# Optimization experiments

Hardware: AMD Instinct MI355X
Metric: run time of the kernel (lower is better)

The kernel has to match this reference:

```python
import jax, jax.numpy as jnp
import numpy as np

N = 250_000          # total event nodes across the batch
E = 1_000_000        # directed edges (radius-graph style, avg degree 4)
B = 25               # graphs in the batch
BS = N // B          # nodes per graph (contiguous blocks)
NX, NY = 8, 9        # ceil(120/16), ceil(100/12) voxel cells for MaxPooling
NC = NX * NY         # 72 voxel cells per graph
M = B * NC           # pooled node slots (empty cells kept but masked)
GRIDS = 16           # MaxPoolingX: 4x4 cells of size (30,25) over 120x100
NOUT = 2
EPS = 1e-5


def spline_basis(p):
    # SplineConv basis: kernel_size=2 per dim, degree=1 open B-spline, dim=3.
    # basis_s(p) = prod_d (p_d if bit_d(s) else 1 - p_d), s = b0 + 2*b1 + 4*b2
    p = jnp.clip(p, 0.0, 1.0)
    cols = []
    for s in range(8):
        w = jnp.ones(p.shape[0], p.dtype)
        for d in range(3):
            w = w * (p[:, d] if (s >> d) & 1 else 1.0 - p[:, d])
        cols.append(w)
    return jnp.stack(cols, axis=1)  # [E, 8]


def spline_conv(x, src, dst, basis, W, emask, num_nodes):
    # SplineConv with aggr='mean', bias=False, root_weight=False
    xj = x[src]                                   # [E, Cin] gather
    msg = jnp.zeros((xj.shape[0], W.shape[2]), x.dtype)
    for s in range(W.shape[0]):                   # 8 kernel weight matrices
        msg = msg + basis[:, s:s + 1] * (xj @ W[s])
    msg = msg * emask[:, None]
    out = jax.ops.segment_sum(msg, dst, num_segments=num_nodes)
    deg = jax.ops.segment_sum(emask, dst, num_segments=num_nodes)
    return out / jnp.maximum(deg, 1.0)[:, None]


def batch_norm(x, gamma, beta, mask=None):
    # BatchNorm1d over nodes (training-mode batch statistics, biased var)
    if mask is None:
        mean = x.mean(axis=0)
        var = jnp.mean((x - mean) ** 2, axis=0)
        return (x - mean) * jax.lax.rsqrt(var + EPS) * gamma + beta
    m = mask.astype(x.dtype)[:, None]
    cnt = jnp.maximum(m.sum(), 1.0)
    mean = (x * m).sum(axis=0) / cnt
    var = (((x - mean) ** 2) * m).sum(axis=0) / cnt
    return ((x - mean) * jax.lax.rsqrt(var + EPS) * gamma + beta) * m


def _forward(x, pos, edge_attr, ws, gs, bs, fc_w, edge_index, batch):
    src, dst = edge_index[0], edge_index[1]
    basis = spline_basis(edge_attr)
    em = jnp.ones((src.shape[0],), x.dtype)
    for i in range(5):  # conv1..conv5 + norm + relu on the full event graph
        x = spline_conv(x, src, dst, basis, ws[i], em, N)
        x = jax.nn.relu(batch_norm(x, gs[i], bs[i]))
    # ---- MaxPooling: voxel grid (16,12) over pos[:, :2], coarsen graph ----
    cx = jnp.clip(jnp.floor(pos[:, 0] / 16.0).astype(jnp.int32), 0, NX - 1)
    cy = jnp.clip(jnp.floor(pos[:, 1] / 12.0).astype(jnp.int32), 0, NY - 1)
    cluster = batch * NC + cy * NX + cx           # [N] -> [0, M)
    cnt = jax.ops.segment_sum(jnp.ones((N,), x.dtype), cluster, num_segments=M)
    nmask = cnt > 0                               # non-empty voxel cells
    xp = jax.ops.segment_max(x, cluster, num_segments=M)
    xp = jnp.where(nmask[:, None], xp, 0.0)       # [M, 32]
    pp = jax.ops.segment_sum(pos, cluster, num_segments=M) / jnp.maximum(cnt, 1.0)[:, None]
    # coarsen edges: remap via cluster, drop self loops, coalesce duplicates
    key = cluster[src] * M + cluster[dst]
    key = jnp.where(cluster[src] == cluster[dst], M * M, key)
    ks = jnp.sort(key)
    dup = jnp.concatenate([jnp.zeros((1,), bool), ks[1:] == ks[:-1]])
    evalid = (ks < M * M) & (~dup)
    rs = jnp.where(evalid, ks // M, 0)
    cs = jnp.where(evalid, ks % M, 0)
    emf = evalid.astype(x.dtype)
    # Cartesian(norm=True, cat=False) on pooled positions
    d = (pp[cs] - pp[rs]) * emf[:, None]
    maxv = jnp.maximum(jnp.max(jnp.abs(d)), 1e-9)
    ea2 = d / (2.0 * maxv) + 0.5
    basis2 = spline_basis(ea2)
    for i in range(5, 7):  # conv6, conv7 on pooled graph
        xp = spline_conv(xp, rs, cs, basis2, ws[i], emf, M)
        xp = jax.nn.relu(batch_norm(xp, gs[i], bs[i], nmask))
    # ---- MaxPoolingX: (30,25) voxel grid -> 4x4 = 16 cells per graph ----
    bcl = jnp.arange(M, dtype=jnp.int32) // NC    # batch id of each cluster
    gx = jnp.clip(jnp.floor(pp[:, 0] / 30.0).astype(jnp.int32), 0, 3)
    gy = jnp.clip(jnp.floor(pp[:, 1] / 25.0).astype(jnp.int32), 0, 3)
    seg = jnp.where(nmask, bcl * GRIDS + gy * 4 + gx, B * GRIDS)
    xg = jax.ops.segment_max(xp, seg, num_segments=B * GRIDS + 1)[:B * GRIDS]
    xg = jnp.where(jnp.isfinite(xg), xg, 0.0)     # empty cells -> 0
    feat = xg.reshape(B, GRIDS * 32)              # [B, 512]
    return feat @ fc_w.T                          # [B, NOUT]


def setup_inputs() -> dict:
    key = jax.random.key(0)
    k = jax.random.split(key, 16)
    x = jax.random.uniform(k[0], (N, 1), dtype=jnp.float32)
    pos = jax.random.uniform(k[1], (N, 3), dtype=jnp.float32) * jnp.array([120.0, 100.0, 1.0], jnp.float32)
    batch = (jnp.arange(N) // BS).astype(jnp.int32)
    src = jax.random.randint(k[2], (E,), 0, N, dtype=jnp.int32)
    dst = (src // BS) * BS + jax.random.randint(k[3], (E,), 0, BS, dtype=jnp.int32)
    edge_index = jnp.stack([src, dst])
    edge_attr = jax.random.uniform(k[4], (E, 3), dtype=jnp.float32)
    chans = [1, 8, 16, 16, 16, 32, 32, 32]
    inp = {"x": x, "pos": pos, "edge_attr": edge_attr}
    for i in range(7):
        cin, cout = chans[i], chans[i + 1]
        inp[f"w{i+1}"] = jax.random.normal(k[5 + i], (8, cin, cout), jnp.float32) / np.sqrt(8.0 * cin)
    for i in range(7):
        inp[f"g{i+1}"] = jnp.ones((chans[i + 1],), jnp.float32)
    for i in range(7):
        inp[f"b{i+1}"] = jnp.zeros((chans[i + 1],), jnp.float32)
    inp["fc_w"] = jax.random.normal(k[12], (NOUT, GRIDS * 32), jnp.float32) * 0.05
    inp["edge_index"] = edge_index
    inp["batch"] = batch
    return inp


def reference(x, pos, edge_attr, w1, w2, w3, w4, w5, w6, w7,
              g1, g2, g3, g4, g5, g6, g7,
              b1, b2, b3, b4, b5, b6, b7, fc_w, edge_index, batch):
    ws = (w1, w2, w3, w4, w5, w6, w7)
    gs = (g1, g2, g3, g4, g5, g6, g7)
    bs = (b1, b2, b3, b4, b5, b6, b7)
    return _forward(x, pos, edge_attr, ws, gs, bs, fc_w, edge_index, batch)
```

## Files before the change

kernel.cpp:

```cpp
#include <hip/hip_runtime.h>

constexpr int NN   = 250000;
constexpr int NE   = 1000000;
constexpr int NBm  = 25;
constexpr int BSg  = NN / NBm;
constexpr int NCc  = 72;
constexpr int MM   = NBm * NCc;
constexpr int PRES = NBm * NCc * NCc;
constexpr int NBK  = NBm * 16;
constexpr float EPSbn = 1e-5f;


__global__ __launch_bounds__(256) void k_deg(const int* __restrict__ dst, int* __restrict__ deg, int n) {
    int e = blockIdx.x * 256 + threadIdx.x;
    if (e < n) atomicAdd(&deg[dst[e]], 1);
}

__global__ __launch_bounds__(256) void k_dhist(const int* __restrict__ deg, const int* __restrict__ batch,
                                               int* __restrict__ dhist, int n) {
    __shared__ int h[NBK];
    int tid = threadIdx.x;
    for (int i = tid; i < NBK; i += 256) h[i] = 0;
    __syncthreads();
    int i = blockIdx.x * 256 + tid;
    if (i < n) atomicAdd(&h[batch[i] * 16 + (15 - min(deg[i], 15))], 1);
    __syncthreads();
    for (int b = tid; b < NBK; b += 256) if (h[b]) atomicAdd(&dhist[b], h[b]);
}

__global__ __launch_bounds__(256) void k_dscan(const int* __restrict__ dhist, int* __restrict__ dcur) {
    __shared__ int tmp[NBK];
    int t = threadIdx.x;
    for (int i = t; i < NBK; i += 256) tmp[i] = dhist[i];
    __syncthreads();
    if (t == 0) { int run = 0; for (int i = 0; i < NBK; i++) { int v = tmp[i]; tmp[i] = run; run += v; } }
    __syncthreads();
    for (int i = t; i < NBK; i += 256) dcur[i] = tmp[i];
}

__global__ __launch_bounds__(256) void k_dscat(const int* __restrict__ deg, const int* __restrict__ batch,
                                               const float* __restrict__ x_in,
                                               int* __restrict__ dcur, int* __restrict__ pinv,
                                               int* __restrict__ deg_p, float* __restrict__ xin_p, int n) {
    __shared__ int lcnt[NBK];
    __shared__ int gbase[NBK];
    int tid = threadIdx.x;
    for (int i = tid; i < NBK; i += 256) lcnt[i] = 0;
    __syncthreads();
    int i = blockIdx.x * 256 + tid;
    int b = 0, rank = 0;
    if (i < n) {
        b = batch[i] * 16 + (15 - min(deg[i], 15));
        rank = atomicAdd(&lcnt[b], 1);
    }
    __syncthreads();
    for (int k = tid; k < NBK; k += 256)
        if (lcnt[k]) gbase[k] = atomicAdd(&dcur[k], lcnt[k]);
    __syncthreads();
    if (i < n) {
        int slot = gbase[b] + rank;
        pinv[i] = slot;
        deg_p[slot] = deg[i];
        xin_p[slot] = x_in[i];
    }
}

__global__ __launch_bounds__(256) void k_scan1(const int* __restrict__ in, int n,
                                               int* __restrict__ outEx, int* __restrict__ bsum) {
    __shared__ int lds[256];
    int t = threadIdx.x;
    int base = blockIdx.x * 2048;
    int v[8]; int s = 0;
#pragma unroll
    for (int i = 0; i < 8; i++) { int idx = base + t * 8 + i; v[i] = (idx < n) ? in[idx] : 0; s += v[i]; }
    lds[t] = s; __syncthreads();
    for (int o = 1; o < 256; o <<= 1) {
        int x = (t >= o) ? lds[t - o] : 0; __syncthreads();
        lds[t] += x; __syncthreads();
    }
    if (t == 255) bsum[blockIdx.x] = lds[255];
    int run = lds[t] - s;
#pragma unroll
    for (int i = 0; i < 8; i++) { int idx = base + t * 8 + i; if (idx < n) outEx[idx] = run; run += v[i]; }
}

__global__ __launch_bounds__(256) void k_scan2(int* bsum, int nb) {
    __shared__ int l[256];
    int t = threadIdx.x;
    int v = (t < nb) ? bsum[t] : 0;
    l[t] = v; __syncthreads();
    for (int o = 1; o < 256; o <<= 1) {
        int x = (t >= o) ? l[t - o] : 0; __syncthreads();
        l[t] += x; __syncthreads();
    }
    if (t < nb) bsum[t] = l[t] - v;
}

__global__ __launch_bounds__(256) void k_scan3(int* __restrict__ outEx, int n, const int* __restrict__ bsum) {
    int i = blockIdx.x * 256 + threadIdx.x;
    if (i < n) outEx[i] += bsum[i >> 11];
}

__global__ __launch_bounds__(256) void k_scatter(const int* __restrict__ src, const int* __restrict__ dst,
                                                 const float* __restrict__ ea, const int* __restrict__ offx,
                                                 const int* __restrict__ pinv,
                                                 int* __restrict__ cursor, float4* __restrict__ erec, int n) {
    int e = blockIdx.x * 256 + threadIdx.x;
    if (e >= n) return;
    int d = pinv[dst[e]];
    int j = offx[d] + atomicAdd(&cursor[d], 1);
    float p0 = fminf(fmaxf(ea[e * 3 + 0], 0.f), 1.f);
    float p1 = fminf(fmaxf(ea[e * 3 + 1], 0.f), 1.f);
    float p2 = fminf(fmaxf(ea[e * 3 + 2], 0.f), 1.f);
    erec[j] = make_float4(__int_as_float(pinv[src[e]]), p0, p1, p2);
}

__global__ __launch_bounds__(256) void k_cluster(const float* __restrict__ pos, const int* __restrict__ batch,
                                                 const int* __restrict__ pinv,
                                                 int* __restrict__ cluster, int* __restrict__ cluster_p,
                                                 int* __restrict__ cnt, float* __restrict__ ppsum, int n) {
    int i = blockIdx.x * 256 + threadIdx.x;
    if (i >= n) return;
    float px = pos[i * 3], py = pos[i * 3 + 1], pz = pos[i * 3 + 2];
    int cx = min(max((int)floorf(px / 16.f), 0), 7);
    int cy = min(max((int)floorf(py / 12.f), 0), 8);
    int cl = batch[i] * NCc + cy * 8 + cx;
    cluster[i] = cl;
    cluster_p[pinv[i]] = cl;
    atomicAdd(&cnt[cl], 1);
    atomicAdd(&ppsum[cl * 3 + 0], px);
    atomicAdd(&ppsum[cl * 3 + 1], py);
    atomicAdd(&ppsum[cl * 3 + 2], pz);
}

__global__ __launch_bounds__(256) void k_coarse(const int* __restrict__ src, const int* __restrict__ dst,
                                                const int* __restrict__ cluster, unsigned char* __restrict__ presence,
                                                int n) {
    int e = blockIdx.x * 256 + threadIdx.x;
    if (e >= n) return;
    int r = cluster[src[e]], c = cluster[dst[e]];
    if (r == c) return;
    int g = r / NCc;
    presence[g * (NCc * NCc) + (r % NCc) * NCc + (c % NCc)] = 1;
}

__global__ __launch_bounds__(256) void k_fpp(const int* __restrict__ cnt, const float* __restrict__ ppsum,
                                             float* __restrict__ pp, int* __restrict__ nmask, int* __restrict__ nmc) {
    int m = blockIdx.x * 256 + threadIdx.x;
    if (m >= MM) return;
    int c = cnt[m];
    float inv = 1.f / (float)max(c, 1);
    pp[m * 3 + 0] = ppsum[m * 3 + 0] * inv;
    pp[m * 3 + 1] = ppsum[m * 3 + 1] * inv;
    pp[m * 3 + 2] = ppsum[m * 3 + 2] * inv;
    nmask[m] = (c > 0);
    if (c > 0) atomicAdd(nmc, 1);
}

__global__ __launch_bounds__(256) void k_maxv(const unsigned char* __restrict__ presence, const float* __restrict__ pp,
                                              float* __restrict__ maxv) {
    int i = blockIdx.x * 256 + threadIdx.x;
    float m = 0.f;
    if (i < PRES && presence[i]) {
        int g = i / (NCc * NCc), rem = i % (NCc * NCc);
        int r = g * NCc + rem / NCc, c = g * NCc + rem % NCc;
        float d0 = fabsf(pp[c * 3 + 0] - pp[r * 3 + 0]);
        float d1 = fabsf(pp[c * 3 + 1] - pp[r * 3 + 1]);
        float d2 = fabsf(pp[c * 3 + 2] - pp[r * 3 + 2]);
        m = fmaxf(fmaxf(d0, d1), d2);
    }
    for (int o = 32; o; o >>= 1) m = fmaxf(m, __shfl_xor(m, o));
    if ((threadIdx.x & 63) == 0) atomicMax((int*)maxv, __float_as_int(m));
}


template <int CIN, int COUT, int TPN, bool BN>
__global__ __launch_bounds__(256) void k_conv(
    const float* __restrict__ x, const float4* __restrict__ erec,
    const int* __restrict__ off, const int* __restrict__ deg,
    const float* __restrict__ W, const float* __restrict__ st,
    const float* __restrict__ gam, const float* __restrict__ bet, float invcnt,
    float* __restrict__ out, float* __restrict__ stG, int nwaves) {
    constexpr int CPT = CIN / TPN;
    constexpr int SLICE = COUT + 4;
    constexpr int NPW = 128 / TPN;
    constexpr int CPG = (BSg + NPW - 1) / NPW;
    constexpr int WPG = (CPG + 1) / 2;
    constexpr int NH = (COUT > 16) ? 2 : 1;
    constexpr int OH = COUT / NH;
    constexpr int CWH = OH / TPN;
    __shared__ float Ws[8 * CIN * SLICE];
    __shared__ float ssum[COUT], ssq[COUT];
    int tid = threadIdx.x;
    for (int idx = tid; idx < 8 * CIN * COUT; idx += 256) {
        int s = idx / (CIN * COUT), r = idx % (CIN * COUT);
        int ci = r / COUT, co = r % COUT;
        int t_ = ci / CPT, i_ = ci % CPT;
        Ws[((s * CPT + i_) * TPN + t_) * SLICE + co] = W[idx];
    }
    if (tid < COUT) { ssum[tid] = 0.f; ssq[tid] = 0.f; }
    __syncthreads();

    int w = blockIdx.x * 4 + (tid >> 6);
    int lane = tid & 63;
    int t = lane & (TPN - 1);
    int qi = lane / TPN;
    bool wact = (w < nwaves);
    int g = wact ? (w / WPG) : 0;
    int p = wact ? (w % WPG) : 0;

    float sc[CPT], sh[CPT];
    if constexpr (BN) {
#pragma unroll
        for (int i = 0; i < CPT; i++) {
            int c = t * CPT + i;
            float mean = st[c] * invcnt;
            float var = st[CIN + c] * invcnt - mean * mean;
            float s = rsqrtf(var + EPSbn) * gam[c];
            sc[i] = s; sh[i] = bet[c] - mean * s;
        }
    }

    for (int rep = 0; rep < 2; rep++) {
        if (!wact) break;
        int c = rep ? (CPG - 1 - p) : p;
        if (rep && c == p) break;
        int base = g * BSg + c * NPW;
        int lim = min(NPW, BSg - c * NPW);
        int no = 2 * qi;
        bool act = no < lim;
        int n0 = base + no;

        float agg[2][8 * CPT];
#pragma unroll
        for (int r = 0; r < 2; r++)
#pragma unroll
            for (int i = 0; i < 8 * CPT; i++) agg[r][i] = 0.f;

        int dgr[2] = {0, 0};
        int jbr[2] = {0, 0};
        if (act) {
            jbr[0] = off[n0];     dgr[0] = deg[n0];
            jbr[1] = off[n0 + 1]; dgr[1] = deg[n0 + 1];
        }
        int mx = max(dgr[0], dgr[1]);
        for (int m = 0; m < mx; m++) {
#pragma unroll
            for (int r = 0; r < 2; r++) {
                if (m < dgr[r]) {
                    float4 rec = erec[jbr[r] + m];
                    int s = __float_as_int(rec.x);
                    float p0 = rec.y, p1 = rec.z, p2 = rec.w;
                    float q0 = 1.f - p0, q1 = 1.f - p1, q2 = 1.f - p2;
                    float a00 = q0 * q1, a10 = p0 * q1, a01 = q0 * p1, a11 = p0 * p1;
                    float bbv[8] = {a00 * q2, a10 * q2, a01 * q2, a11 * q2,
                                    a00 * p2, a10 * p2, a01 * p2, a11 * p2};
                    const float* xs = &x[(size_t)s * CIN + t * CPT];
                    float xv[CPT];
                    if constexpr (CPT == 4) {
                        float4 v = *(const float4*)xs;
                        xv[0] = v.x; xv[1] = v.y; xv[2] = v.z; xv[3] = v.w;
                    } else {
#pragma unroll
                        for (int i = 0; i < CPT; i++) xv[i] = xs[i];
                    }
                    if constexpr (BN) {
#pragma unroll
                        for (int i = 0; i < CPT; i++) { float v = xv[i] * sc[i] + sh[i]; xv[i] = v > 0.f ? v : 0.f; }
                    }
#pragma unroll
                    for (int k = 0; k < 8; k++)
#pragma unroll
                        for (int i = 0; i < CPT; i++) agg[r][k * CPT + i] += bbv[k] * xv[i];
                }
            }
        }

        float inv0 = 1.f / (float)max(dgr[0], 1);
        float inv1 = 1.f / (float)max(dgr[1], 1);

#pragma unroll
        for (int h = 0; h < NH; h++) {
            float o0[OH], o1[OH];
#pragma unroll
            for (int c2 = 0; c2 < OH; c2++) { o0[c2] = 0.f; o1[c2] = 0.f; }
#pragma unroll
            for (int k = 0; k < 8; k++)
#pragma unroll
                for (int i = 0; i < CPT; i++) {
                    float a0 = agg[0][k * CPT + i];
                    float a1 = agg[1][k * CPT + i];
                    const float4* wr = (const float4*)&Ws[((k * CPT + i) * TPN + t) * SLICE + h * OH];
#pragma unroll
                    for (int c2 = 0; c2 < OH / 4; c2++) {
                        float4 wv = wr[c2];
                        o0[4 * c2 + 0] += a0 * wv.x; o0[4 * c2 + 1] += a0 * wv.y;
                        o0[4 * c2 + 2] += a0 * wv.z; o0[4 * c2 + 3] += a0 * wv.w;
                        o1[4 * c2 + 0] += a1 * wv.x; o1[4 * c2 + 1] += a1 * wv.y;
                        o1[4 * c2 + 2] += a1 * wv.z; o1[4 * c2 + 3] += a1 * wv.w;
                    }
                }
#pragma unroll
            for (int m = 1; m < TPN; m <<= 1)
#pragma unroll
                for (int c2 = 0; c2 < OH; c2++) { o0[c2] += __shfl_xor(o0[c2], m); o1[c2] += __shfl_xor(o1[c2], m); }

            float v0[CWH], v1[CWH], sv[CWH], qv[CWH];
#pragma unroll
            for (int c2 = 0; c2 < CWH; c2++) {
                v0[c2] = act ? o0[t * CWH + c2] * inv0 : 0.f;
                v1[c2] = act ? o1[t * CWH + c2] * inv1 : 0.f;
                sv[c2] = v0[c2] + v1[c2];
                qv[c2] = v0[c2] * v0[c2] + v1[c2] * v1[c2];
            }
            if (act) {
                float* op0 = &out[(size_t)n0 * COUT + h * OH + t * CWH];
                float* op1 = op0 + COUT;
#pragma unroll
                for (int c2 = 0; c2 < CWH; c2++) { op0[c2] = v0[c2]; op1[c2] = v1[c2]; }
            }
#pragma unroll
            for (int m = TPN; m < 64; m <<= 1)
#pragma unroll
                for (int c2 = 0; c2 < CWH; c2++) { sv[c2] += __shfl_xor(sv[c2], m); qv[c2] += __shfl_xor(qv[c2], m); }
            if (lane < TPN) {
#pragma unroll
                for (int c2 = 0; c2 < CWH; c2++) {
                    atomicAdd(&ssum[h * OH + t * CWH + c2], sv[c2]);
                    atomicAdd(&ssq[h * OH + t * CWH + c2], qv[c2]);
                }
            }
        }
    }
    __syncthreads();
    if (tid < COUT) atomicAdd(&stG[tid], ssum[tid]);
    else if (tid < 2 * COUT) atomicAdd(&stG[tid], ssq[tid - COUT]);
}

template <int C>
__global__ __launch_bounds__(256) void k_stats(const float* __restrict__ x, int rows, float* __restrict__ st) {
    __shared__ float ls[256], lq[256];
    int t = threadIdx.x;
    int gid = blockIdx.x * 256 + t;
    int c = t % C;
    int r0 = gid / C;
    int rstride = (gridDim.x * 256) / C;
    float s = 0.f, q = 0.f;
    for (int r = r0; r < rows; r += rstride) { float v = x[(size_t)r * C + c]; s += v; q += v * v; }
    ls[t] = s; lq[t] = q;
    __syncthreads();
    if (t < C) {
        float ss = 0.f, qq = 0.f;
        for (int k = t; k < 256; k += C) { ss += ls[k]; qq += lq[k]; }
        atomicAdd(&st[c], ss); atomicAdd(&st[C + c], qq);
    }
}

__global__ __launch_bounds__(256) void k_pool(const float* __restrict__ x, const int* __restrict__ cluster_p,
                                              const float* __restrict__ st, const float* __restrict__ gam,
                                              const float* __restrict__ bet, float invcnt,
                                              float* __restrict__ xp) {
    __shared__ float cellv[NCc * 32];
    __shared__ float scs[32], shs[32];
    int tid = threadIdx.x;
    int g = (blockIdx.x & 7) + 8 * (blockIdx.x >> 6);
    int part = (blockIdx.x >> 3) & 7;
    for (int i = tid; i < NCc * 32; i += 256) cellv[i] = 0.f;
    if (tid < 32) {
        float mean = st[tid] * invcnt;
        float var = st[32 + tid] * invcnt - mean * mean;
        float s = rsqrtf(var + EPSbn) * gam[tid];
        scs[tid] = s; shs[tid] = bet[tid] - mean * s;
    }
    __syncthreads();
    if (g < NBm) {
        int base = g * BSg + part * (BSg / 8);
        const int nelem = (BSg / 8) * 32;
        for (int ii = tid; ii < nelem; ii += 256) {
            int nd = base + (ii >> 5), ch = ii & 31;
            float v = x[(size_t)nd * 32 + ch] * scs[ch] + shs[ch];
            v = v > 0.f ? v : 0.f;
            int lc = cluster_p[nd] - g * NCc;
            atomicMax((int*)&cellv[lc * 32 + ch], __float_as_int(v));
        }
        __syncthreads();
        for (int ii = tid; ii < NCc * 32; ii += 256)
            atomicMax((int*)&xp[g * NCc * 32 + ii], __float_as_int(cellv[ii]));
    }
}

__global__ __launch_bounds__(256) void k_y(const float* __restrict__ xp, const float* __restrict__ W,
                                           float* __restrict__ y) {
    int i = blockIdx.x * 256 + threadIdx.x;
    if (i >= MM * 256) return;
    int r = i >> 8, rem = i & 255, s = rem >> 5, co = rem & 31;
    const float* xr = &xp[r * 32];
    const float* w = &W[s * 1024 + co];
    float a = 0.f;
#pragma unroll
    for (int ci = 0; ci < 32; ci++) a += xr[ci] * w[ci * 32];
    y[i] = a;
}

__global__ __launch_bounds__(256) void k_convp(const float* __restrict__ y, const float* __restrict__ pp,
                                               const unsigned char* __restrict__ presence,
                                               const float* __restrict__ maxv, float* __restrict__ out) {
    int i = blockIdx.x * 256 + threadIdx.x;
    if (i >= MM * 32) return;
    int c = i >> 5, co = i & 31;
    int g = c / NCc, lc = c % NCc;
    float mv = fmaxf(maxv[0], 1e-9f);
    float inv2 = 0.5f / mv;
    float pcx = pp[c * 3], pcy = pp[c * 3 + 1], pcz = pp[c * 3 + 2];
    const unsigned char* pr = &presence[g * (NCc * NCc) + lc];
    float acc = 0.f; int dg = 0;
    for (int lr = 0; lr < NCc; lr++) {
        if (pr[lr * NCc]) {
            dg++;
            int r = g * NCc + lr;
            float p0 = fminf(fmaxf((pcx - pp[r * 3]) * inv2 + 0.5f, 0.f), 1.f);
            float p1 = fminf(fmaxf((pcy - pp[r * 3 + 1]) * inv2 + 0.5f, 0.f), 1.f);
            float p2 = fminf(fmaxf((pcz - pp[r * 3 + 2]) * inv2 + 0.5f, 0.f), 1.f);
            float q0 = 1.f - p0, q1 = 1.f - p1, q2 = 1.f - p2;
            const float* yr = &y[r * 256 + co];
            acc += (q0 * q1 * q2) * yr[0]   + (p0 * q1 * q2) * yr[32]
                 + (q0 * p1 * q2) * yr[64]  + (p0 * p1 * q2) * yr[96]
                 + (q0 * q1 * p2) * yr[128] + (p0 * q1 * p2) * yr[160]
                 + (q0 * p1 * p2) * yr[192] + (p0 * p1 * p2) * yr[224];
        }
    }
    out[i] = acc / (float)max(dg, 1);
}

__global__ __launch_bounds__(256) void k_bnp(float* __restrict__ xp, const float* __restrict__ st,
                                             const float* __restrict__ gam, const float* __restrict__ bet,
                                             const int* __restrict__ nmask, const int* __restrict__ nmc) {
    int i = blockIdx.x * 256 + threadIdx.x;
    if (i >= MM * 32) return;
    int m = i >> 5, ch = i & 31;
    float cnt = (float)max(nmc[0], 1);
    float mean = st[ch] / cnt;
    float var = st[32 + ch] / cnt - mean * mean;
    float s = rsqrtf(var + EPSbn) * gam[ch];
    float v = xp[i] * s + (bet[ch] - mean * s);
    v = v > 0.f ? v : 0.f;
    xp[i] = nmask[m] ? v : 0.f;
}

__global__ __launch_bounds__(256) void k_poolX(const float* __restrict__ xp, const float* __restrict__ pp,
                                               const int* __restrict__ nmask, float* __restrict__ xg) {
    int i = blockIdx.x * 256 + threadIdx.x;
    if (i >= MM * 32) return;
    int m = i >> 5, ch = i & 31;
    if (!nmask[m]) return;
    int g = m / NCc;
    int gx = min(max((int)floorf(pp[m * 3] / 30.f), 0), 3);
    int gy = min(max((int)floorf(pp[m * 3 + 1] / 25.f), 0), 3);
    int seg = g * 16 + gy * 4 + gx;
    atomicMax((int*)&xg[seg * 32 + ch], __float_as_int(xp[i]));
}

__global__ __launch_bounds__(64) void k_fc(const float* __restrict__ xg, const float* __restrict__ fcw,
                                           float* __restrict__ out) {
    int q = blockIdx.x;
    int b = q >> 1, o = q & 1;
    int l = threadIdx.x;
    float a = 0.f;
    for (int k = l; k < 512; k += 64) a += xg[b * 512 + k] * fcw[o * 512 + k];
    for (int s = 32; s; s >>= 1) a += __shfl_xor(a, s);
    if (l == 0) out[b * 2 + o] = a;
}


extern "C" void kernel_launch(void* const* d_in, const int* in_sizes, int n_in,
                              void* d_out, int out_size, void* d_ws, size_t ws_size,
                              hipStream_t stream) {
    const float* x_in  = (const float*)d_in[0];
    const float* pos   = (const float*)d_in[1];
    const float* eattr = (const float*)d_in[2];
    const float* w[7];  for (int i = 0; i < 7; i++) w[i]  = (const float*)d_in[3 + i];
    const float* gm[7]; for (int i = 0; i < 7; i++) gm[i] = (const float*)d_in[10 + i];
    const float* bt[7]; for (int i = 0; i < 7; i++) bt[i] = (const float*)d_in[17 + i];
    const float* fcw   = (const float*)d_in[24];
    const int* ei      = (const int*)d_in[25];
    const int* batch   = (const int*)d_in[26];
    const int* esrc = ei;
    const int* edst = ei + NE;
    float* outp = (float*)d_out;

    char* base = (char*)d_ws;
    size_t cur = 0;
    auto alloc = [&](size_t elems) -> void* {
        void* p = base + cur;
        cur += (((elems * 4) + 255) & ~(size_t)255);
        return p;
    };
    int*   deg_i     = (int*)alloc(NN);
    int*   cursor    = (int*)alloc(NN);
    int*   cnt_i     = (int*)alloc(MM);
    float* ppsum     = (float*)alloc(MM * 3);
    unsigned char* presence = (unsigned char*)alloc(PRES / 4);
    float* maxv      = (float*)alloc(64);
    int*   nmc       = (int*)alloc(64);
    int*   dhist     = (int*)alloc(NBK);
    float* st        = (float*)alloc(7 * 64);
    float* xp_pool   = (float*)alloc(MM * 32);
    float* xg        = (float*)alloc(NBm * 16 * 32);
    size_t zero_bytes = cur;
    int*   off_ex    = (int*)alloc(NN);
    int*   bsum      = (int*)alloc(256);
    int*   cluster   = (int*)alloc(NN);
    int*   cluster_p = (int*)alloc(NN);
    int*   dcur      = (int*)alloc(NBK);
    int*   pinv      = (int*)alloc(NN);
    int*   deg_p     = (int*)alloc(NN);
    float* xin_p     = (float*)alloc(NN);
    float4* erec     = (float4*)alloc((size_t)NE * 4);
    float* x_a       = (float*)alloc((size_t)NN * 32);
    float* x_b       = (float*)alloc((size_t)NN * 16);
    float* pp        = (float*)alloc(MM * 3);
    int*   nmask     = (int*)alloc(MM);
    float* ybuf      = (float*)alloc(MM * 256);
    float* pt0       = (float*)alloc(MM * 32);
    float* pt1       = (float*)alloc(MM * 32);
    (void)ws_size; (void)in_sizes; (void)n_in; (void)out_size;

    (void)hipMemsetAsync(d_ws, 0, zero_bytes, stream);

    int gE = (NE + 255) / 256;
    int gN = (NN + 255) / 256;
    int nbS = (NN + 2047) / 2048;

    k_deg<<<gE, 256, 0, stream>>>(edst, deg_i, NE);
    k_dhist<<<gN, 256, 0, stream>>>(deg_i, batch, dhist, NN);
    k_dscan<<<1, 256, 0, stream>>>(dhist, dcur);
    k_dscat<<<gN, 256, 0, stream>>>(deg_i, batch, x_in, dcur, pinv, deg_p, xin_p, NN);
    k_scan1<<<nbS, 256, 0, stream>>>(deg_p, NN, off_ex, bsum);
    k_scan2<<<1, 256, 0, stream>>>(bsum, nbS);
    k_scan3<<<gN, 256, 0, stream>>>(off_ex, NN, bsum);
    k_scatter<<<gE, 256, 0, stream>>>(esrc, edst, eattr, off_ex, pinv, cursor, erec, NE);
    k_cluster<<<gN, 256, 0, stream>>>(pos, batch, pinv, cluster, cluster_p, cnt_i, ppsum, NN);
    k_coarse<<<gE, 256, 0, stream>>>(esrc, edst, cluster, presence, NE);
    k_fpp<<<(MM + 255) / 256, 256, 0, stream>>>(cnt_i, ppsum, pp, nmask, nmc);
    k_maxv<<<(PRES + 255) / 256, 256, 0, stream>>>(presence, pp, maxv);

    const float invN = 1.f / (float)NN;
    constexpr int W1 = NBm * ((((BSg + 127) / 128) + 1) / 2);
    constexpr int W2 = NBm * ((((BSg + 63) / 64) + 1) / 2);
    constexpr int W4 = NBm * ((((BSg + 31) / 32) + 1) / 2);
    k_conv<1, 8, 1, false><<<(W1 + 3) / 4, 256, 0, stream>>>(xin_p, erec, off_ex, deg_p,
                                                             w[0], nullptr, nullptr, nullptr, 0.f, x_a, st + 0, W1);
    k_conv<8, 16, 2, true><<<(W2 + 3) / 4, 256, 0, stream>>>(x_a, erec, off_ex, deg_p,
                                                             w[1], st + 0, gm[0], bt[0], invN, x_b, st + 64, W2);
    k_conv<16, 16, 4, true><<<(W4 + 3) / 4, 256, 0, stream>>>(x_b, erec, off_ex, deg_p,
                                                              w[2], st + 64, gm[1], bt[1], invN, x_a, st + 128, W4);
    k_conv<16, 16, 4, true><<<(W4 + 3) / 4, 256, 0, stream>>>(x_a, erec, off_ex, deg_p,
                                                              w[3], st + 128, gm[2], bt[2], invN, x_b, st + 192, W4);
    k_conv<16, 32, 4, true><<<(W4 + 3) / 4, 256, 0, stream>>>(x_b, erec, off_ex, deg_p,
                                                              w[4], st + 192, gm[3], bt[3], invN, x_a, st + 256, W4);
    k_pool<<<256, 256, 0, stream>>>(x_a, cluster_p, st + 256, gm[4], bt[4], invN, xp_pool);
    k_y<<<(MM * 256 + 255) / 256, 256, 0, stream>>>(xp_pool, w[5], ybuf);
    k_convp<<<(MM * 32 + 255) / 256, 256, 0, stream>>>(ybuf, pp, presence, maxv, pt0);
    k_stats<32><<<8, 256, 0, stream>>>(pt0, MM, st + 320);
    k_bnp<<<(MM * 32 + 255) / 256, 256, 0, stream>>>(pt0, st + 320, gm[5], bt[5], nmask, nmc);
    k_y<<<(MM * 256 + 255) / 256, 256, 0, stream>>>(pt0, w[6], ybuf);
    k_convp<<<(MM * 32 + 255) / 256, 256, 0, stream>>>(ybuf, pp, presence, maxv, pt1);
    k_stats<32><<<8, 256, 0, stream>>>(pt1, MM, st + 384);
    k_bnp<<<(MM * 32 + 255) / 256, 256, 0, stream>>>(pt1, st + 384, gm[6], bt[6], nmask, nmc);
    k_poolX<<<(MM * 32 + 255) / 256, 256, 0, stream>>>(pt1, pp, nmask, xg);
    k_fc<<<50, 64, 0, stream>>>(xg, fcw, outp);
}
```

Baseline: 747.1 us.

## Interleave conv blocks across graphs and branchlessly pair edge gathers

The conv kernels now map block indices so that consecutive blocks come from different graphs (8 graphs interleaved), with fixed grid sizes. This is likely meant to spread work and memory traffic across XCDs or channels. The inner edge loop no longer branches per node: it issues both edge-record and feature gathers together, using clamped indices and zero-weight masking, to raise memory-level parallelism. The cost is redundant loads and FMAs for the shorter-degree node, and the hardcoded grid sizes must cover all waves.

```diff
diff --git a/kernel.cpp b/kernel.cpp
--- a/kernel.cpp
+++ b/kernel.cpp
@@ -180,12 +180,13 @@
     const int* __restrict__ off, const int* __restrict__ deg,
     const float* __restrict__ W, const float* __restrict__ st,
     const float* __restrict__ gam, const float* __restrict__ bet, float invcnt,
-    float* __restrict__ out, float* __restrict__ stG, int nwaves) {
+    float* __restrict__ out, float* __restrict__ stG) {
     constexpr int CPT = CIN / TPN;
     constexpr int SLICE = COUT + 4;
     constexpr int NPW = 128 / TPN;
     constexpr int CPG = (BSg + NPW - 1) / NPW;
     constexpr int WPG = (CPG + 1) / 2;
+    constexpr int BPGc = (WPG + 3) / 4;
     constexpr int NH = (COUT > 16) ? 2 : 1;
     constexpr int OH = COUT / NH;
     constexpr int CWH = OH / TPN;
@@ -201,13 +202,13 @@
     if (tid < COUT) { ssum[tid] = 0.f; ssq[tid] = 0.f; }
     __syncthreads();
 
-    int w = blockIdx.x * 4 + (tid >> 6);
+    int g = (blockIdx.x & 7) + 8 * ((blockIdx.x >> 3) / BPGc);
+    int lb = (blockIdx.x >> 3) % BPGc;
+    int p = lb * 4 + (tid >> 6);
     int lane = tid & 63;
     int t = lane & (TPN - 1);
     int qi = lane / TPN;
-    bool wact = (w < nwaves);
-    int g = wact ? (w / WPG) : 0;
-    int p = wact ? (w % WPG) : 0;
+    bool wact = (g < NBm) && (p < WPG);
 
     float sc[CPT], sh[CPT];
     if constexpr (BN) {
@@ -237,47 +238,68 @@
 #pragma unroll
             for (int i = 0; i < 8 * CPT; i++) agg[r][i] = 0.f;
 
-        int dgr[2] = {0, 0};
-        int jbr[2] = {0, 0};
+        int dg0 = 0, dg1 = 0, jb0 = 0, jb1 = 0;
         if (act) {
-            jbr[0] = off[n0];     dgr[0] = deg[n0];
-            jbr[1] = off[n0 + 1]; dgr[1] = deg[n0 + 1];
+            jb0 = off[n0];     dg0 = deg[n0];
+            jb1 = off[n0 + 1]; dg1 = deg[n0 + 1];
         }
-        int mx = max(dgr[0], dgr[1]);
+        int mx = max(dg0, dg1);
         for (int m = 0; m < mx; m++) {
-#pragma unroll
-            for (int r = 0; r < 2; r++) {
-                if (m < dgr[r]) {
-                    float4 rec = erec[jbr[r] + m];
-                    int s = __float_as_int(rec.x);
-                    float p0 = rec.y, p1 = rec.z, p2 = rec.w;
-                    float q0 = 1.f - p0, q1 = 1.f - p1, q2 = 1.f - p2;
-                    float a00 = q0 * q1, a10 = p0 * q1, a01 = q0 * p1, a11 = p0 * p1;
-                    float bbv[8] = {a00 * q2, a10 * q2, a01 * q2, a11 * q2,
-                                    a00 * p2, a10 * p2, a01 * p2, a11 * p2};
-                    const float* xs = &x[(size_t)s * CIN + t * CPT];
-                    float xv[CPT];
-                    if constexpr (CPT == 4) {
-                        float4 v = *(const float4*)xs;
-                        xv[0] = v.x; xv[1] = v.y; xv[2] = v.z; xv[3] = v.w;
-                    } else {
-#pragma unroll
-                        for (int i = 0; i < CPT; i++) xv[i] = xs[i];
-                    }
-                    if constexpr (BN) {
-#pragma unroll
-                        for (int i = 0; i < CPT; i++) { float v = xv[i] * sc[i] + sh[i]; xv[i] = v > 0.f ? v : 0.f; }
-                    }
-#pragma unroll
-                    for (int k = 0; k < 8; k++)
-#pragma unroll
-                        for (int i = 0; i < CPT; i++) agg[r][k * CPT + i] += bbv[k] * xv[i];
+            int j0 = jb0 + max(min(m, dg0 - 1), 0);
+            int j1 = jb1 + max(min(m, dg1 - 1), 0);
+            float4 rec0 = erec[j0];
+            float4 rec1 = erec[j1];
+            float f0 = (m < dg0) ? 1.f : 0.f;
+            float f1 = (m < dg1) ? 1.f : 0.f;
+            int s0 = __float_as_int(rec0.x);
+            int s1 = __float_as_int(rec1.x);
+            float xv0[CPT], xv1[CPT];
+            const float* xs0 = &x[(size_t)s0 * CIN + t * CPT];
+            const float* xs1 = &x[(size_t)s1 * CIN + t * CPT];
+            if constexpr (CPT == 4) {
+                float4 v0 = *(const float4*)xs0;
+                float4 v1 = *(const float4*)xs1;
+                xv0[0] = v0.x; xv0[1] = v0.y; xv0[2] = v0.z; xv0[3] = v0.w;
+                xv1[0] = v1.x; xv1[1] = v1.y; xv1[2] = v1.z; xv1[3] = v1.w;
+            } else {
+#pragma unroll
+                for (int i = 0; i < CPT; i++) { xv0[i] = xs0[i]; xv1[i] = xs1[i]; }
+            }
+            if constexpr (BN) {
+#pragma unroll
+                for (int i = 0; i < CPT; i++) {
+                    float a = xv0[i] * sc[i] + sh[i]; xv0[i] = a > 0.f ? a : 0.f;
+                    float b = xv1[i] * sc[i] + sh[i]; xv1[i] = b > 0.f ? b : 0.f;
                 }
             }
+            {
+                float p0 = rec0.y, p1 = rec0.z;
+                float p2 = rec0.w * f0, q2 = (1.f - rec0.w) * f0;
+                float q0 = 1.f - p0, q1 = 1.f - p1;
+                float a00 = q0 * q1, a10 = p0 * q1, a01 = q0 * p1, a11 = p0 * p1;
+                float bbv[8] = {a00 * q2, a10 * q2, a01 * q2, a11 * q2,
+                                a00 * p2, a10 * p2, a01 * p2, a11 * p2};
+#pragma unroll
+                for (int k = 0; k < 8; k++)
+#pragma unroll
+                    for (int i = 0; i < CPT; i++) agg[0][k * CPT + i] += bbv[k] * xv0[i];
+            }
+            {
+                float p0 = rec1.y, p1 = rec1.z;
+                float p2 = rec1.w * f1, q2 = (1.f - rec1.w) * f1;
+                float q0 = 1.f - p0, q1 = 1.f - p1;
+                float a00 = q0 * q1, a10 = p0 * q1, a01 = q0 * p1, a11 = p0 * p1;
+                float bbv[8] = {a00 * q2, a10 * q2, a01 * q2, a11 * q2,
+                                a00 * p2, a10 * p2, a01 * p2, a11 * p2};
+#pragma unroll
+                for (int k = 0; k < 8; k++)
+#pragma unroll
+                    for (int i = 0; i < CPT; i++) agg[1][k * CPT + i] += bbv[k] * xv1[i];
+            }
         }
 
-        float inv0 = 1.f / (float)max(dgr[0], 1);
-        float inv1 = 1.f / (float)max(dgr[1], 1);
+        float inv0 = 1.f / (float)max(dg0, 1);
+        float inv1 = 1.f / (float)max(dg1, 1);
 
 #pragma unroll
         for (int h = 0; h < NH; h++) {
@@ -545,19 +567,16 @@
     k_maxv<<<(PRES + 255) / 256, 256, 0, stream>>>(presence, pp, maxv);
 
     const float invN = 1.f / (float)NN;
-    constexpr int W1 = NBm * ((((BSg + 127) / 128) + 1) / 2);
-    constexpr int W2 = NBm * ((((BSg + 63) / 64) + 1) / 2);
-    constexpr int W4 = NBm * ((((BSg + 31) / 32) + 1) / 2);
-    k_conv<1, 8, 1, false><<<(W1 + 3) / 4, 256, 0, stream>>>(xin_p, erec, off_ex, deg_p,
-                                                             w[0], nullptr, nullptr, nullptr, 0.f, x_a, st + 0, W1);
-    k_conv<8, 16, 2, true><<<(W2 + 3) / 4, 256, 0, stream>>>(x_a, erec, off_ex, deg_p,
-                                                             w[1], st + 0, gm[0], bt[0], invN, x_b, st + 64, W2);
-    k_conv<16, 16, 4, true><<<(W4 + 3) / 4, 256, 0, stream>>>(x_b, erec, off_ex, deg_p,
-                                                              w[2], st + 64, gm[1], bt[1], invN, x_a, st + 128, W4);
-    k_conv<16, 16, 4, true><<<(W4 + 3) / 4, 256, 0, stream>>>(x_a, erec, off_ex, deg_p,
-                                                              w[3], st + 128, gm[2], bt[2], invN, x_b, st + 192, W4);
-    k_conv<16, 32, 4, true><<<(W4 + 3) / 4, 256, 0, stream>>>(x_b, erec, off_ex, deg_p,
-                                                              w[4], st + 192, gm[3], bt[3], invN, x_a, st + 256, W4);
+    k_conv<1, 8, 1, false><<<320, 256, 0, stream>>>(xin_p, erec, off_ex, deg_p,
+                                                    w[0], nullptr, nullptr, nullptr, 0.f, x_a, st + 0);
+    k_conv<8, 16, 2, true><<<640, 256, 0, stream>>>(x_a, erec, off_ex, deg_p,
+                                                    w[1], st + 0, gm[0], bt[0], invN, x_b, st + 64);
+    k_conv<16, 16, 4, true><<<1280, 256, 0, stream>>>(x_b, erec, off_ex, deg_p,
+                                                      w[2], st + 64, gm[1], bt[1], invN, x_a, st + 128);
+    k_conv<16, 16, 4, true><<<1280, 256, 0, stream>>>(x_a, erec, off_ex, deg_p,
+                                                      w[3], st + 128, gm[2], bt[2], invN, x_b, st + 192);
+    k_conv<16, 32, 4, true><<<1280, 256, 0, stream>>>(x_b, erec, off_ex, deg_p,
+                                                      w[4], st + 192, gm[3], bt[3], invN, x_a, st + 256);
     k_pool<<<256, 256, 0, stream>>>(x_a, cluster_p, st + 256, gm[4], bt[4], invN, xp_pool);
     k_y<<<(MM * 256 + 255) / 256, 256, 0, stream>>>(xp_pool, w[5], ybuf);
     k_convp<<<(MM * 32 + 255) / 256, 256, 0, stream>>>(ybuf, pp, presence, maxv, pt0);
```

Measured after the change: 736.3 us. No clear change (-1.4%).
